# Kernel tuning notes

Hardware: AMD Instinct MI355X
Metric: run time of the kernel (lower is better)

Reference implementation:

```python
import jax, jax.numpy as jnp
import numpy as np

HBLK = 16  # hadamard / nvfp4 block size
FP4_LEVELS = jnp.array([0.0, 0.5, 1.0, 1.5, 2.0, 3.0, 4.0, 6.0], dtype=jnp.float32)
FP4_MIDS = jnp.array([0.25, 0.75, 1.25, 1.75, 2.5, 3.5, 5.0], dtype=jnp.float32)


def _hadamard(n):
    H = np.array([[1.0]])
    while H.shape[0] < n:
        H = np.block([[H, H], [H, -H]])
    return jnp.asarray(H / np.sqrt(n), dtype=jnp.float32)  # orthonormal

H16 = _hadamard(HBLK)


def rht_forward(x, signs):
    # x: [M, K], K % 16 == 0 (no padding needed). Random sign diag then block Hadamard.
    M, K = x.shape
    xb = x.reshape(M, K // HBLK, HBLK)
    return ((xb * signs) @ H16).reshape(M, K)


def q_emulate(x):
    # NVFP4 quantize->dequantize along last dim: blocks of 16, E4M3 block scale = amax/6,
    # round-to-nearest onto E2M1 grid {0,.5,1,1.5,2,3,4,6} (signed).
    M, K = x.shape
    xb = x.reshape(M, K // HBLK, HBLK)
    amax = jnp.max(jnp.abs(xb), axis=-1, keepdims=True)
    scale = (amax / 6.0).astype(jnp.float8_e4m3fn).astype(x.dtype)
    safe = jnp.where(scale == 0, 1.0, scale)
    a = jnp.clip(jnp.abs(xb) / safe, 0.0, 6.0)
    q = FP4_LEVELS[jnp.searchsorted(FP4_MIDS, a)]
    return (jnp.sign(xb) * q * scale).reshape(M, K)


def setup_inputs() -> dict:
    key = jax.random.key(0)
    kx, kw, kb, ks1, ks2 = jax.random.split(key, 5)
    IN, OUT = 4096, 4096
    x = jax.random.normal(kx, (4, 2048, IN), dtype=jnp.float32)
    weight = jax.random.normal(kw, (OUT, IN), dtype=jnp.float32) / np.sqrt(IN)
    bound = 1.0 / np.sqrt(IN)
    bias = jax.random.uniform(kb, (OUT,), dtype=jnp.float32, minval=-bound, maxval=bound)
    signs_in = jnp.where(jax.random.bernoulli(ks1, 0.5, (HBLK,)), 1.0, -1.0).astype(jnp.float32)
    signs_grad = jnp.where(jax.random.bernoulli(ks2, 0.5, (HBLK,)), 1.0, -1.0).astype(jnp.float32)
    return {"x": x, "weight": weight, "bias": bias, "signs_in": signs_in, "signs_grad": signs_grad}


def reference(x, weight, bias, signs_in, signs_grad):
    # signs_grad only used in backward (kept for interface parity).
    x_flat = x.reshape(-1, x.shape[-1])
    x_q = q_emulate(rht_forward(x_flat, signs_in))
    w_q = q_emulate(rht_forward(weight, signs_in))
    y = x_q @ w_q.T + bias
    return y.reshape(*x.shape[:-1], weight.shape[0])
```

## Files before the change

kernel.cpp:

```cpp
#include <hip/hip_runtime.h>
#include <stdint.h>


typedef __bf16 bf16x8 __attribute__((ext_vector_type(8)));
typedef float f32x4 __attribute__((ext_vector_type(4)));


__device__ __forceinline__ float e4m3_rt(float x) {
    unsigned int u = __float_as_uint(x);
    int ex = (int)((u >> 23) & 0xffu) - 127;
    if (ex < -6) ex = -6;
    float qs = __uint_as_float((unsigned)(127 + 3 - ex) << 23);
    float qi = __uint_as_float((unsigned)(127 + ex - 3) << 23);
    return rintf(x * qs) * qi;
}

__device__ __forceinline__ unsigned pack2(float lo, float hi) {
    return (__float_as_uint(lo) >> 16) | (__float_as_uint(hi) & 0xFFFF0000u);
}

__global__ __launch_bounds__(256) void quant_rht_kernel(
    const float* __restrict__ X, const float* __restrict__ signs,
    uint16_t* __restrict__ Q, int ngroups)
{
    int gid = blockIdx.x * 256 + threadIdx.x;
    if (gid >= ngroups) return;

    const float4* p = (const float4*)(X + (size_t)gid * 16);
    float4 v0 = p[0], v1 = p[1], v2 = p[2], v3 = p[3];
    const float4* sp = (const float4*)signs;
    float4 s0 = sp[0], s1 = sp[1], s2 = sp[2], s3 = sp[3];

    float t0 = v0.x * s0.x, t1 = v0.y * s0.y, t2 = v0.z * s0.z, t3 = v0.w * s0.w;
    float t4 = v1.x * s1.x, t5 = v1.y * s1.y, t6 = v1.z * s1.z, t7 = v1.w * s1.w;
    float t8 = v2.x * s2.x, t9 = v2.y * s2.y, t10 = v2.z * s2.z, t11 = v2.w * s2.w;
    float t12 = v3.x * s3.x, t13 = v3.y * s3.y, t14 = v3.z * s3.z, t15 = v3.w * s3.w;

#define BT(a, b) { float _s = (a) + (b), _d = (a) - (b); (a) = _s; (b) = _d; }
    BT(t0,t1)  BT(t2,t3)  BT(t4,t5)   BT(t6,t7)
    BT(t8,t9)  BT(t10,t11) BT(t12,t13) BT(t14,t15)
    BT(t0,t2)  BT(t1,t3)  BT(t4,t6)   BT(t5,t7)
    BT(t8,t10) BT(t9,t11) BT(t12,t14) BT(t13,t15)
    BT(t0,t4)  BT(t1,t5)  BT(t2,t6)   BT(t3,t7)
    BT(t8,t12) BT(t9,t13) BT(t10,t14) BT(t11,t15)
    BT(t0,t8)  BT(t1,t9)  BT(t2,t10)  BT(t3,t11)
    BT(t4,t12) BT(t5,t13) BT(t6,t14)  BT(t7,t15)
#undef BT

    t0 *= 0.25f;  t1 *= 0.25f;  t2 *= 0.25f;  t3 *= 0.25f;
    t4 *= 0.25f;  t5 *= 0.25f;  t6 *= 0.25f;  t7 *= 0.25f;
    t8 *= 0.25f;  t9 *= 0.25f;  t10 *= 0.25f; t11 *= 0.25f;
    t12 *= 0.25f; t13 *= 0.25f; t14 *= 0.25f; t15 *= 0.25f;

    float amax = fmaxf(
        fmaxf(fmaxf(fmaxf(fabsf(t0), fabsf(t1)), fmaxf(fabsf(t2), fabsf(t3))),
              fmaxf(fmaxf(fabsf(t4), fabsf(t5)), fmaxf(fabsf(t6), fabsf(t7)))),
        fmaxf(fmaxf(fmaxf(fabsf(t8), fabsf(t9)), fmaxf(fabsf(t10), fabsf(t11))),
              fmaxf(fmaxf(fabsf(t12), fabsf(t13)), fmaxf(fabsf(t14), fabsf(t15)))));

    float scale = e4m3_rt(amax / 6.0f);
    float safe = (scale == 0.0f) ? 1.0f : scale;

    float m1 = 0.25f * safe, m2 = 0.75f * safe, m3 = 1.25f * safe,
          m4 = 1.75f * safe, m5 = 2.5f * safe,  m6 = 3.5f * safe,
          m7 = 5.0f * safe;

#define Q1(tv) ({                                                              \
    float _a = fabsf(tv);                                                      \
    float _q = _a > m5 ? (_a > m7 ? 6.0f : (_a > m6 ? 4.0f : 3.0f))            \
                       : (_a > m3 ? (_a > m4 ? 2.0f : 1.5f)                    \
                                  : (_a > m2 ? 1.0f : (_a > m1 ? 0.5f : 0.0f)));\
    copysignf(_q * scale, (tv)); })

    unsigned w0 = pack2(Q1(t0),  Q1(t1));
    unsigned w1 = pack2(Q1(t2),  Q1(t3));
    unsigned w2 = pack2(Q1(t4),  Q1(t5));
    unsigned w3 = pack2(Q1(t6),  Q1(t7));
    unsigned w4 = pack2(Q1(t8),  Q1(t9));
    unsigned w5 = pack2(Q1(t10), Q1(t11));
    unsigned w6 = pack2(Q1(t12), Q1(t13));
    unsigned w7 = pack2(Q1(t14), Q1(t15));
#undef Q1

    uint4* q4 = (uint4*)(Q + (size_t)gid * 16);
    q4[0] = make_uint4(w0, w1, w2, w3);
    q4[1] = make_uint4(w4, w5, w6, w7);
}


#define BM 256
#define BN 256

__global__ __launch_bounds__(512, 2) void gemm_bt_bias(
    const uint16_t* __restrict__ A,
    const uint16_t* __restrict__ B,
    const float* __restrict__ bias,
    float* __restrict__ C,
    int M, int N, int K)
{
    __shared__ uint4 sh[8][1024];

    const int tid  = threadIdx.x;
    const int lane = tid & 63;
    const int wave = tid >> 6;
    const int wm = wave >> 2, wn = wave & 3;
    const int lm = lane & 15, g4 = lane >> 4;
    const int bn = blockIdx.x, bm = blockIdx.y;

    const int NT  = K >> 6;
    const int NHT = NT << 2;

    const int p0 = tid, p1 = 512 + tid;
    const int c0 = p0 ^ ((p0 >> 3) & 7);
    const int c1 = p1 ^ ((p1 >> 3) & 7);
    const uint16_t* asrc0 = A + (size_t)(bm * BM + (c0 >> 2)) * K + (c0 & 3) * 8;
    const uint16_t* asrc1 = A + (size_t)(bm * BM + (c1 >> 2)) * K + (c1 & 3) * 8;
    const uint16_t* bsrc0 = B + (size_t)(bn * BN + (c0 >> 2)) * K + (c0 & 3) * 8;
    const uint16_t* bsrc1 = B + (size_t)(bn * BN + (c1 >> 2)) * K + (c1 & 3) * 8;
    char* ldsd0 = (char*)&sh[0][0] + p0 * 16;
    char* ldsd1 = (char*)&sh[0][0] + p1 * 16;

    int aPos[8], bPos[4];
#pragma unroll
    for (int f = 0; f < 8; ++f) {
        int c = (wm * 128 + f * 16 + lm) * 4 + g4;
        aPos[f] = c ^ ((c >> 3) & 7);
    }
#pragma unroll
    for (int f = 0; f < 4; ++f) {
        int c = (wn * 64 + f * 16 + lm) * 4 + g4;
        bPos[f] = c ^ ((c >> 3) & 7);
    }

    f32x4 acc[8][4];
#pragma unroll
    for (int i = 0; i < 8; ++i)
#pragma unroll
        for (int j = 0; j < 4; ++j) acc[i][j] = (f32x4){0.f, 0.f, 0.f, 0.f};

    bf16x8 a0[4], a1[4], b0[4], b1[4];

#define STAGE(jj) do {                                                        \
    int _j = (jj);                                                            \
    int _koff = (_j < NHT) ? (((_j >> 2) << 6) | (((_j >> 1) & 1) << 5)) : 0; \
    int _sb = (_j & 7) << 14;                                                 \
    const uint16_t* _s0 = (_j & 1) ? bsrc0 : asrc0;                           \
    const uint16_t* _s1 = (_j & 1) ? bsrc1 : asrc1;                           \
    __builtin_amdgcn_global_load_lds(                                         \
        (const __attribute__((address_space(1))) unsigned int*)(_s0 + _koff), \
        (__attribute__((address_space(3))) unsigned int*)(ldsd0 + _sb),       \
        16, 0, 0);                                                            \
    __builtin_amdgcn_global_load_lds(                                         \
        (const __attribute__((address_space(1))) unsigned int*)(_s1 + _koff), \
        (__attribute__((address_space(3))) unsigned int*)(ldsd1 + _sb),       \
        16, 0, 0);                                                            \
} while (0)

#define WIN(ARH, CA, CB, NA, NSA, NRH, LOADB, NB, NSB, SJ, GATE) do {         \
    __builtin_amdgcn_s_setprio(1);                                            \
    _Pragma("unroll")                                                         \
    for (int _i = 0; _i < 4; ++_i)                                            \
        _Pragma("unroll")                                                     \
        for (int _jj = 0; _jj < 4; ++_jj)                                     \
            acc[4*(ARH) + _i][_jj] = __builtin_amdgcn_mfma_f32_16x16x32_bf16( \
                CA[_i], CB[_jj], acc[4*(ARH) + _i][_jj], 0, 0, 0);            \
    __builtin_amdgcn_s_setprio(0);                                            \
    _Pragma("unroll")                                                         \
    for (int _i = 0; _i < 4; ++_i)                                            \
        NA[_i] = __builtin_bit_cast(bf16x8, sh[NSA][aPos[4*(NRH) + _i]]);     \
    if (LOADB) {                                                              \
        _Pragma("unroll")                                                     \
        for (int _jj = 0; _jj < 4; ++_jj)                                     \
            NB[_jj] = __builtin_bit_cast(bf16x8, sh[NSB][bPos[_jj]]);         \
    }                                                                         \
    STAGE(hb + (SJ));                                                         \
    if (GATE) asm volatile("s_waitcnt vmcnt(6)" ::: "memory");                \
    __builtin_amdgcn_sched_barrier(0);                                        \
    __builtin_amdgcn_s_barrier();                                             \
} while (0)

    STAGE(0); STAGE(1); STAGE(2); STAGE(3); STAGE(4); STAGE(5);
    asm volatile("s_waitcnt vmcnt(8)" ::: "memory");
    __builtin_amdgcn_s_barrier();
#pragma unroll
    for (int i = 0; i < 4; ++i)
        a1[i] = __builtin_bit_cast(bf16x8, sh[0][aPos[i]]);
#pragma unroll
    for (int j = 0; j < 4; ++j)
        b0[j] = __builtin_bit_cast(bf16x8, sh[1][bPos[j]]);

    const int NT2 = NT >> 1;
    for (int it2 = 0; it2 < NT2; ++it2) {
        const int hb = it2 << 3;
        WIN(0, a1, b0, a0, 0, 1, 0, b1, 0,  6, 1);
        WIN(1, a0, b0, a1, 2, 0, 1, b1, 3,  7, 0);
        WIN(0, a1, b1, a0, 2, 1, 0, b0, 0,  8, 1);
        WIN(1, a0, b1, a1, 4, 0, 1, b0, 5,  9, 0);
        WIN(0, a1, b0, a0, 4, 1, 0, b1, 0, 10, 1);
        WIN(1, a0, b0, a1, 6, 0, 1, b1, 7, 11, 0);
        WIN(0, a1, b1, a0, 6, 1, 0, b0, 0, 12, 1);
        WIN(1, a0, b1, a1, 0, 0, 1, b0, 1, 13, 0);
    }
    asm volatile("s_waitcnt vmcnt(0) lgkmcnt(0)" ::: "memory");

#undef WIN
#undef STAGE

#pragma unroll
    for (int j = 0; j < 4; ++j) {
        int col = bn * BN + wn * 64 + j * 16 + lm;
        float bj = bias[col];
#pragma unroll
        for (int i = 0; i < 8; ++i) {
            int row0 = bm * BM + wm * 128 + i * 16 + g4 * 4;
#pragma unroll
            for (int r = 0; r < 4; ++r) {
                C[(size_t)(row0 + r) * (size_t)N + col] = acc[i][j][r] + bj;
            }
        }
    }
}


extern "C" void kernel_launch(void* const* d_in, const int* in_sizes, int n_in,
                              void* d_out, int out_size, void* d_ws, size_t ws_size,
                              hipStream_t stream)
{
    const float* x        = (const float*)d_in[0];
    const float* w        = (const float*)d_in[1];
    const float* bias     = (const float*)d_in[2];
    const float* signs_in = (const float*)d_in[3];

    const int OUT = in_sizes[2];
    const int IN  = in_sizes[1] / OUT;
    const int M   = in_sizes[0] / IN;

    uint16_t* xq = (uint16_t*)d_ws;
    uint16_t* wq = xq + (size_t)M * (size_t)IN;
    (void)ws_size; (void)n_in; (void)out_size;

    int ngx = (int)((size_t)M * IN / 16);
    int ngw = (int)((size_t)OUT * IN / 16);
    quant_rht_kernel<<<(ngx + 255) / 256, 256, 0, stream>>>(x, signs_in, xq, ngx);
    quant_rht_kernel<<<(ngw + 255) / 256, 256, 0, stream>>>(w, signs_in, wq, ngw);

    dim3 grid(OUT / BN, M / BM);
    gemm_bt_bias<<<grid, 512, 0, stream>>>(xq, wq, bias, (float*)d_out, M, OUT, IN);
}
```

Before: 473.4 us.

## Restructure GEMM pipeline to full-K-tile double buffering and fuse quant kernels

The two RHT quantization launches become one grid-stride kernel that handles both activations and weights, removing a launch and its tail. The GEMM main loop swaps the fine-grained 8-slot half-tile staging scheme for two LDS buffers that each hold a full 64-wide K tile. A whole tile's fragments are prefetched into a double-buffered register set while the previous tile's MFMAs run. Each window ends with a full vmcnt(0)/lgkmcnt(0) wait plus a barrier, so global-load latency is hidden only by one window of MFMAs. The much larger fragment register arrays raise register pressure under launch_bounds(512,2) and risk spills or lower occupancy.

```diff
diff --git a/kernel.cpp b/kernel.cpp
--- a/kernel.cpp
+++ b/kernel.cpp
@@ -4,6 +4,9 @@
 
 typedef __bf16 bf16x8 __attribute__((ext_vector_type(8)));
 typedef float f32x4 __attribute__((ext_vector_type(4)));
+
+#define AS1 __attribute__((address_space(1)))
+#define AS3 __attribute__((address_space(3)))
 
 
 __device__ __forceinline__ float e4m3_rt(float x) {
@@ -19,17 +22,12 @@
     return (__float_as_uint(lo) >> 16) | (__float_as_uint(hi) & 0xFFFF0000u);
 }
 
-__global__ __launch_bounds__(256) void quant_rht_kernel(
-    const float* __restrict__ X, const float* __restrict__ signs,
-    uint16_t* __restrict__ Q, int ngroups)
-{
-    int gid = blockIdx.x * 256 + threadIdx.x;
-    if (gid >= ngroups) return;
-
-    const float4* p = (const float4*)(X + (size_t)gid * 16);
+__device__ __forceinline__ void quant_group(const float* __restrict__ src,
+                                            uint16_t* __restrict__ dst,
+                                            float4 s0, float4 s1, float4 s2, float4 s3)
+{
+    const float4* p = (const float4*)src;
     float4 v0 = p[0], v1 = p[1], v2 = p[2], v3 = p[3];
-    const float4* sp = (const float4*)signs;
-    float4 s0 = sp[0], s1 = sp[1], s2 = sp[2], s3 = sp[3];
 
     float t0 = v0.x * s0.x, t1 = v0.y * s0.y, t2 = v0.z * s0.z, t3 = v0.w * s0.w;
     float t4 = v1.x * s1.x, t5 = v1.y * s1.y, t6 = v1.z * s1.z, t7 = v1.w * s1.w;
@@ -82,9 +80,29 @@
     unsigned w7 = pack2(Q1(t14), Q1(t15));
 #undef Q1
 
-    uint4* q4 = (uint4*)(Q + (size_t)gid * 16);
+    uint4* q4 = (uint4*)dst;
     q4[0] = make_uint4(w0, w1, w2, w3);
     q4[1] = make_uint4(w4, w5, w6, w7);
+}
+
+__global__ __launch_bounds__(256) void quant_rht_fused(
+    const float* __restrict__ X, const float* __restrict__ W,
+    const float* __restrict__ signs,
+    uint16_t* __restrict__ QX, uint16_t* __restrict__ QW,
+    int ngx, int ngtot)
+{
+    const float4* sp = (const float4*)signs;
+    float4 s0 = sp[0], s1 = sp[1], s2 = sp[2], s3 = sp[3];
+
+    for (int gid = blockIdx.x * 256 + threadIdx.x; gid < ngtot;
+         gid += gridDim.x * 256) {
+        if (gid < ngx)
+            quant_group(X + (size_t)gid * 16, QX + (size_t)gid * 16, s0, s1, s2, s3);
+        else {
+            size_t g = (size_t)(gid - ngx);
+            quant_group(W + g * 16, QW + g * 16, s0, s1, s2, s3);
+        }
+    }
 }
 
 
@@ -107,8 +125,7 @@
     const int lm = lane & 15, g4 = lane >> 4;
     const int bn = blockIdx.x, bm = blockIdx.y;
 
-    const int NT  = K >> 6;
-    const int NHT = NT << 2;
+    const int NT = K >> 6;
 
     const int p0 = tid, p1 = 512 + tid;
     const int c0 = p0 ^ ((p0 >> 3) & 7);
@@ -138,73 +155,79 @@
 #pragma unroll
         for (int j = 0; j < 4; ++j) acc[i][j] = (f32x4){0.f, 0.f, 0.f, 0.f};
 
-    bf16x8 a0[4], a1[4], b0[4], b1[4];
-
-#define STAGE(jj) do {                                                        \
-    int _j = (jj);                                                            \
-    int _koff = (_j < NHT) ? (((_j >> 2) << 6) | (((_j >> 1) & 1) << 5)) : 0; \
-    int _sb = (_j & 7) << 14;                                                 \
-    const uint16_t* _s0 = (_j & 1) ? bsrc0 : asrc0;                           \
-    const uint16_t* _s1 = (_j & 1) ? bsrc1 : asrc1;                           \
-    __builtin_amdgcn_global_load_lds(                                         \
-        (const __attribute__((address_space(1))) unsigned int*)(_s0 + _koff), \
-        (__attribute__((address_space(3))) unsigned int*)(ldsd0 + _sb),       \
-        16, 0, 0);                                                            \
-    __builtin_amdgcn_global_load_lds(                                         \
-        (const __attribute__((address_space(1))) unsigned int*)(_s1 + _koff), \
-        (__attribute__((address_space(3))) unsigned int*)(ldsd1 + _sb),       \
-        16, 0, 0);                                                            \
+    bf16x8 aF[2][2][8];
+    bf16x8 bF[2][2][4];
+
+#define STAGE_P(PAR, T2) do {                                                 \
+    int _ko = ((T2) < NT) ? (T2) * 64 : 0;                                    \
+    const int _sb = (4 * (PAR)) * 16384;                                      \
+    __builtin_amdgcn_global_load_lds((const AS1 unsigned*)(asrc0 + _ko),      \
+        (AS3 unsigned*)(ldsd0 + _sb), 16, 0, 0);                              \
+    __builtin_amdgcn_global_load_lds((const AS1 unsigned*)(asrc1 + _ko),      \
+        (AS3 unsigned*)(ldsd1 + _sb), 16, 0, 0);                              \
+    __builtin_amdgcn_global_load_lds((const AS1 unsigned*)(bsrc0 + _ko),      \
+        (AS3 unsigned*)(ldsd0 + _sb + 16384), 16, 0, 0);                      \
+    __builtin_amdgcn_global_load_lds((const AS1 unsigned*)(bsrc1 + _ko),      \
+        (AS3 unsigned*)(ldsd1 + _sb + 16384), 16, 0, 0);                      \
+    __builtin_amdgcn_global_load_lds((const AS1 unsigned*)(asrc0 + _ko + 32), \
+        (AS3 unsigned*)(ldsd0 + _sb + 32768), 16, 0, 0);                      \
+    __builtin_amdgcn_global_load_lds((const AS1 unsigned*)(asrc1 + _ko + 32), \
+        (AS3 unsigned*)(ldsd1 + _sb + 32768), 16, 0, 0);                      \
+    __builtin_amdgcn_global_load_lds((const AS1 unsigned*)(bsrc0 + _ko + 32), \
+        (AS3 unsigned*)(ldsd0 + _sb + 49152), 16, 0, 0);                      \
+    __builtin_amdgcn_global_load_lds((const AS1 unsigned*)(bsrc1 + _ko + 32), \
+        (AS3 unsigned*)(ldsd1 + _sb + 49152), 16, 0, 0);                      \
 } while (0)
 
-#define WIN(ARH, CA, CB, NA, NSA, NRH, LOADB, NB, NSB, SJ, GATE) do {         \
+#define READS(NB, NPAR) do {                                                  \
+    _Pragma("unroll")                                                         \
+    for (int _f = 0; _f < 8; ++_f) {                                          \
+        aF[NB][0][_f] = __builtin_bit_cast(bf16x8, sh[4*(NPAR)+0][aPos[_f]]); \
+        aF[NB][1][_f] = __builtin_bit_cast(bf16x8, sh[4*(NPAR)+2][aPos[_f]]); \
+    }                                                                         \
+    _Pragma("unroll")                                                         \
+    for (int _j = 0; _j < 4; ++_j) {                                          \
+        bF[NB][0][_j] = __builtin_bit_cast(bf16x8, sh[4*(NPAR)+1][bPos[_j]]); \
+        bF[NB][1][_j] = __builtin_bit_cast(bf16x8, sh[4*(NPAR)+3][bPos[_j]]); \
+    }                                                                         \
+} while (0)
+
+#define WINDOW(CB, PAR, T) do {                                               \
+    STAGE_P(PAR, (T) + 2);                                                    \
+    READS(1 - (CB), 1 - (PAR));                                               \
     __builtin_amdgcn_s_setprio(1);                                            \
     _Pragma("unroll")                                                         \
-    for (int _i = 0; _i < 4; ++_i)                                            \
+    for (int _kh = 0; _kh < 2; ++_kh)                                         \
         _Pragma("unroll")                                                     \
-        for (int _jj = 0; _jj < 4; ++_jj)                                     \
-            acc[4*(ARH) + _i][_jj] = __builtin_amdgcn_mfma_f32_16x16x32_bf16( \
-                CA[_i], CB[_jj], acc[4*(ARH) + _i][_jj], 0, 0, 0);            \
+        for (int _i = 0; _i < 8; ++_i)                                        \
+            _Pragma("unroll")                                                 \
+            for (int _jj = 0; _jj < 4; ++_jj)                                 \
+                acc[_i][_jj] = __builtin_amdgcn_mfma_f32_16x16x32_bf16(       \
+                    aF[CB][_kh][_i], bF[CB][_kh][_jj], acc[_i][_jj], 0, 0, 0);\
     __builtin_amdgcn_s_setprio(0);                                            \
-    _Pragma("unroll")                                                         \
-    for (int _i = 0; _i < 4; ++_i)                                            \
-        NA[_i] = __builtin_bit_cast(bf16x8, sh[NSA][aPos[4*(NRH) + _i]]);     \
-    if (LOADB) {                                                              \
-        _Pragma("unroll")                                                     \
-        for (int _jj = 0; _jj < 4; ++_jj)                                     \
-            NB[_jj] = __builtin_bit_cast(bf16x8, sh[NSB][bPos[_jj]]);         \
-    }                                                                         \
-    STAGE(hb + (SJ));                                                         \
-    if (GATE) asm volatile("s_waitcnt vmcnt(6)" ::: "memory");                \
+    asm volatile("s_waitcnt vmcnt(0) lgkmcnt(0)" ::: "memory");               \
     __builtin_amdgcn_sched_barrier(0);                                        \
     __builtin_amdgcn_s_barrier();                                             \
 } while (0)
 
-    STAGE(0); STAGE(1); STAGE(2); STAGE(3); STAGE(4); STAGE(5);
+    STAGE_P(0, 0);
+    STAGE_P(1, 1);
     asm volatile("s_waitcnt vmcnt(8)" ::: "memory");
     __builtin_amdgcn_s_barrier();
-#pragma unroll
-    for (int i = 0; i < 4; ++i)
-        a1[i] = __builtin_bit_cast(bf16x8, sh[0][aPos[i]]);
-#pragma unroll
-    for (int j = 0; j < 4; ++j)
-        b0[j] = __builtin_bit_cast(bf16x8, sh[1][bPos[j]]);
-
-    const int NT2 = NT >> 1;
-    for (int it2 = 0; it2 < NT2; ++it2) {
-        const int hb = it2 << 3;
-        WIN(0, a1, b0, a0, 0, 1, 0, b1, 0,  6, 1);
-        WIN(1, a0, b0, a1, 2, 0, 1, b1, 3,  7, 0);
-        WIN(0, a1, b1, a0, 2, 1, 0, b0, 0,  8, 1);
-        WIN(1, a0, b1, a1, 4, 0, 1, b0, 5,  9, 0);
-        WIN(0, a1, b0, a0, 4, 1, 0, b1, 0, 10, 1);
-        WIN(1, a0, b0, a1, 6, 0, 1, b1, 7, 11, 0);
-        WIN(0, a1, b1, a0, 6, 1, 0, b0, 0, 12, 1);
-        WIN(1, a0, b1, a1, 0, 0, 1, b0, 1, 13, 0);
-    }
+    READS(0, 0);
     asm volatile("s_waitcnt vmcnt(0) lgkmcnt(0)" ::: "memory");
-
-#undef WIN
-#undef STAGE
+    __builtin_amdgcn_sched_barrier(0);
+    __builtin_amdgcn_s_barrier();
+
+    for (int t = 0; t < NT; t += 2) {
+        WINDOW(0, 0, t);
+        WINDOW(1, 1, t + 1);
+    }
+    asm volatile("s_waitcnt vmcnt(0) lgkmcnt(0)" ::: "memory");
+
+#undef WINDOW
+#undef READS
+#undef STAGE_P
 
 #pragma unroll
     for (int j = 0; j < 4; ++j) {
@@ -241,8 +264,8 @@
 
     int ngx = (int)((size_t)M * IN / 16);
     int ngw = (int)((size_t)OUT * IN / 16);
-    quant_rht_kernel<<<(ngx + 255) / 256, 256, 0, stream>>>(x, signs_in, xq, ngx);
-    quant_rht_kernel<<<(ngw + 255) / 256, 256, 0, stream>>>(w, signs_in, wq, ngw);
+    int ngtot = ngx + ngw;
+    quant_rht_fused<<<2048, 256, 0, stream>>>(x, w, signs_in, xq, wq, ngx, ngtot);
 
     dim3 grid(OUT / BN, M / BM);
     gemm_bt_bias<<<grid, 512, 0, stream>>>(xq, wq, bias, (float*)d_out, M, OUT, IN);
```

After: 1.818 ms. +283.9%, slower.
